# Performance work log

Hardware: AMD Instinct MI355X
Metric: run time of the kernel (lower is better)

## Reference

```python
import jax, jax.numpy as jnp
import numpy as np

V, H, B, T = 32000, 1024, 64, 512
EPS = 1e-5


def setup_inputs() -> dict:
    key = jax.random.key(0)
    ks = jax.random.split(key, 12)
    s = lambda i, shape: (jax.random.normal(ks[i], shape, dtype=jnp.float32) * 0.02)
    inp = {
        "x": jax.random.randint(ks[0], (B, T), 0, V),
        "t": jax.random.uniform(ks[1], (B,), dtype=jnp.float32),
        "emb": s(2, (V, H)),
        "w_ih1": s(3, (4 * H, H)), "w_hh1": s(4, (4 * H, H)),
        "b_ih1": jnp.zeros((4 * H,), jnp.float32), "b_hh1": jnp.zeros((4 * H,), jnp.float32),
        "gamma1": jnp.ones((H,), jnp.float32), "beta1": jnp.zeros((H,), jnp.float32),
        "w_ih2": s(5, (4 * H, H)), "w_hh2": s(6, (4 * H, H)),
        "b_ih2": jnp.zeros((4 * H,), jnp.float32), "b_hh2": jnp.zeros((4 * H,), jnp.float32),
        "gamma2": jnp.ones((H,), jnp.float32), "beta2": jnp.zeros((H,), jnp.float32),
        "fc_w": s(7, (1, H)), "fc_b": jnp.zeros((1,), jnp.float32),
        # LockedDropout: one mask per layer, reused at every timestep, pre-scaled by 1/keep
        "mask1": jax.random.bernoulli(ks[8], 0.5, (B, H)).astype(jnp.float32) / 0.5,
        "mask2": jax.random.bernoulli(ks[9], 0.7, (B, H)).astype(jnp.float32) / 0.7,
    }
    return inp


def _lstm_step(xt, h, c, w_ih, w_hh, b_ih, b_hh):
    # PyTorch LSTMCell gate order: i, f, g, o
    g = xt @ w_ih.T + h @ w_hh.T + (b_ih + b_hh)
    i, f, gg, o = jnp.split(g, 4, axis=-1)
    c = jax.nn.sigmoid(f) * c + jax.nn.sigmoid(i) * jnp.tanh(gg)
    h = jax.nn.sigmoid(o) * jnp.tanh(c)
    return h, c


def _bn(x, gamma, beta):
    # BatchNorm1d in training mode: per-feature batch stats (biased variance)
    m = x.mean(0)
    v = x.var(0)
    return gamma * (x - m) * jax.lax.rsqrt(v + EPS) + beta


def reference(x, t, emb, w_ih1, w_hh1, b_ih1, b_hh1, gamma1, beta1,
              w_ih2, w_hh2, b_ih2, b_hh2, gamma2, beta2, fc_w, fc_b,
              mask1, mask2):
    e = emb[x]                      # [B, T, H]
    e = jnp.transpose(e, (1, 0, 2)) # [T, B, H]

    def step(carry, et):
        h1, c1, h2, c2 = carry
        h1, c1 = _lstm_step(et, h1, c1, w_ih1, w_hh1, b_ih1, b_hh1)
        o = _bn(h1, gamma1, beta1) * mask1
        h2, c2 = _lstm_step(o, h2, c2, w_ih2, w_hh2, b_ih2, b_hh2)
        o = _bn(h2, gamma2, beta2) * mask2
        return (h1, c1, h2, c2), o

    z = jnp.zeros((B, H), jnp.float32)
    _, outs = jax.lax.scan(step, (z, z, z, z), e)  # outs: [T, B, H]

    pooled = outs.max(axis=0)                      # MaxPool1d over time -> [B, H]
    logits = (pooled @ fc_w.T + fc_b)[:, 0]        # [B]
    # BCEWithLogitsLoss (mean), numerically stable
    loss = jnp.mean(jnp.maximum(logits, 0.0) - logits * t + jnp.log1p(jnp.exp(-jnp.abs(logits))))
    return (loss, logits)
```

## Files before the change

### kernel.cpp

```cpp
#include <hip/hip_runtime.h>

#define HDIM  1024
#define BDIM  64
#define TDIM  512
#define FRAGB 131072
#define FRAGE 65536
#define WPAD  1032
#define SLOTS 4
#define NGRP  8

typedef __bf16 bf16x8 __attribute__((ext_vector_type(8)));
typedef float  f32x4  __attribute__((ext_vector_type(4)));
typedef int    i32x4  __attribute__((ext_vector_type(4)));

#define MFMA(a, b, c) __builtin_amdgcn_mfma_f32_16x16x32_bf16(a, b, c, 0, 0, 0)

#define GL(dst, p, off) \
    asm volatile("global_load_dwordx4 %0, %1, off offset:" off " sc0 sc1" \
                 : "=v"(dst) : "v"(p) : "memory")
#define GLF16(f, p) do { \
    const char* p0_ = (const char*)(p); \
    const char* p1_ = p0_ + 4096; const char* p2_ = p0_ + 8192; const char* p3_ = p0_ + 12288; \
    GL(f[0],  p0_, "0"); GL(f[1],  p0_, "1024"); GL(f[2],  p0_, "2048"); GL(f[3],  p0_, "3072"); \
    GL(f[4],  p1_, "0"); GL(f[5],  p1_, "1024"); GL(f[6],  p1_, "2048"); GL(f[7],  p1_, "3072"); \
    GL(f[8],  p2_, "0"); GL(f[9],  p2_, "1024"); GL(f[10], p2_, "2048"); GL(f[11], p2_, "3072"); \
    GL(f[12], p3_, "0"); GL(f[13], p3_, "1024"); GL(f[14], p3_, "2048"); GL(f[15], p3_, "3072"); \
} while (0)
#define WAITV() asm volatile("s_waitcnt vmcnt(0)" ::: "memory")
#define GS16(p, v) \
    asm volatile("global_store_dwordx4 %0, %1, off sc0 sc1" :: "v"(p), "v"(v) : "memory")

__device__ __forceinline__ float sigf(float x) { return 1.0f / (1.0f + expf(-x)); }

__device__ __forceinline__ bf16x8 cvt8(const float* p) {
    const f32x4* q = (const f32x4*)p;
    f32x4 a = q[0], b = q[1];
    bf16x8 r;
    r[0] = (__bf16)a[0]; r[1] = (__bf16)a[1]; r[2] = (__bf16)a[2]; r[3] = (__bf16)a[3];
    r[4] = (__bf16)b[0]; r[5] = (__bf16)b[1]; r[6] = (__bf16)b[2]; r[7] = (__bf16)b[3];
    return r;
}

__device__ __forceinline__ void spin2x8(const int* a, const int* b) {
    if (threadIdx.x < 64) {
        int l = threadIdx.x;
        const int* p = nullptr;
        if (l < 8)       { if (a) p = a + l * 16; }
        else if (l < 16) { if (b) p = b + (l - 8) * 16; }
        for (;;) {
            int v = 16;
            if (p) v = __hip_atomic_load(p, __ATOMIC_RELAXED, __HIP_MEMORY_SCOPE_AGENT);
            if (__all(v >= 16)) break;
            __builtin_amdgcn_s_sleep(1);
        }
    }
    __syncthreads();
}
__device__ __forceinline__ void arrive16(int* sub) {
    WAITV();
    __syncthreads();
    if (threadIdx.x == 0)
        __hip_atomic_fetch_add(sub, 1, __ATOMIC_RELAXED, __HIP_MEMORY_SCOPE_AGENT);
}
__device__ __forceinline__ void spin1(const int* c, int n) {
    if (threadIdx.x == 0)
        while (__hip_atomic_load(c, __ATOMIC_RELAXED, __HIP_MEMORY_SCOPE_AGENT) < n)
            __builtin_amdgcn_s_sleep(1);
    __syncthreads();
}

__global__ void gather_emb(const int* __restrict__ x, const float* __restrict__ emb,
                           __bf16* __restrict__ xseqfrag) {
    int t = blockIdx.x;
    for (int u = threadIdx.x; u < 8192; u += 256) {
        int lane = u & 63, c = (u >> 6) & 31, bt = u >> 11;
        int row = lane & 15, quad = lane >> 4;
        int b = bt * 16 + row, k = c * 32 + quad * 8;
        int tok = x[b * TDIM + t];
        bf16x8 r = cvt8(emb + (size_t)tok * HDIM + k);
        *(bf16x8*)(xseqfrag + (size_t)t * FRAGE + (size_t)u * 8) = r;
    }
}

__global__ void __launch_bounds__(512, 1) rnn_all(
    const int* __restrict__ x, const float* __restrict__ tv,
    const float* __restrict__ emb,
    const float* __restrict__ w_ih1, const float* __restrict__ w_hh1,
    const float* __restrict__ b_ih1, const float* __restrict__ b_hh1,
    const float* __restrict__ gamma1, const float* __restrict__ beta1,
    const float* __restrict__ w_ih2, const float* __restrict__ w_hh2,
    const float* __restrict__ b_ih2, const float* __restrict__ b_hh2,
    const float* __restrict__ gamma2, const float* __restrict__ beta2,
    const float* __restrict__ fc_w, const float* __restrict__ fc_b,
    const float* __restrict__ mask1, const float* __restrict__ mask2,
    const __bf16* __restrict__ xseq, int use_xseq,
    int* __restrict__ l1s, int* __restrict__ l2s, int* __restrict__ poolg,
    char* __restrict__ h1frag, char* __restrict__ h2frag,
    char* __restrict__ o1frag, float* __restrict__ pooled,
    float* __restrict__ out) {
    __shared__ __bf16 wih_s[32 * WPAD];
    __shared__ __bf16 whh_s[32 * WPAD];
    __shared__ float bias_s[32];
    __shared__ float gbuf[64 * 36];
    __shared__ float xh[8 * 68];
    __shared__ float stat_m[8], stat_r[8];
    __shared__ __align__(16) __bf16 hstage[512];
    __shared__ __align__(16) __bf16 ostage[512];

    const int tid   = threadIdx.x;
    const int layer = blockIdx.x & 1;
    const int lb    = blockIdx.x >> 1;
    const int grp   = lb >> 4;
    const int fbase = lb * 8;

    const float* w_ih = layer ? w_ih2 : w_ih1;
    const float* w_hh = layer ? w_hh2 : w_hh1;
    const float* b_ih = layer ? b_ih2 : b_ih1;
    const float* b_hh = layer ? b_hh2 : b_hh1;
    const float* gam_ = layer ? gamma2 : gamma1;
    const float* bet_ = layer ? beta2  : beta1;
    const float* msk_ = layer ? mask2  : mask1;

    for (int idx = tid; idx < 32 * HDIM; idx += 512) {
        int n = idx >> 10, k = idx & 1023;
        int row = (n >> 3) * HDIM + fbase + (n & 7);
        wih_s[n * WPAD + k] = (__bf16)w_ih[row * HDIM + k];
        whh_s[n * WPAD + k] = (__bf16)w_hh[row * HDIM + k];
    }
    if (tid < 32) {
        int row = (tid >> 3) * HDIM + fbase + (tid & 7);
        bias_s[tid] = b_ih[row] + b_hh[row];
    }
    __syncthreads();

    const int lane = tid & 63;
    const int wv   = tid >> 6;
    const int bt   = wv & 3;
    const int kh   = wv >> 2;
    const int qm   = lane & 15;
    const int quad = lane >> 4;
    const int kbase = kh * 512 + quad * 8;
    const int fragoff = ((bt * 32 + kh * 16) * 64 + lane) * 16;

    const __bf16* bwi0 = wih_s + qm * WPAD + kbase;
    const __bf16* bwi1 = wih_s + (16 + qm) * WPAD + kbase;
    const __bf16* bwh0 = whh_s + qm * WPAD + kbase;
    const __bf16* bwh1 = whh_s + (16 + qm) * WPAD + kbase;

    const int bb = tid >> 3, jj = tid & 7;
    const int feat = fbase + jj;
    const float gv = gam_[feat], bev = bet_[feat], mv = msk_[bb * HDIM + feat];
    float c = 0.0f, pmax = -1e30f;

    const int sbb  = tid & 63;
    const int soff = (((sbb >> 4) * 32 + (lb >> 2)) * 64 + ((lb & 3) * 16 + (sbb & 15))) * 16;

#pragma unroll 1
    for (int t = 0; t < TDIM; t++) {
        f32x4 ax0 = {0.f,0.f,0.f,0.f}, ax1 = {0.f,0.f,0.f,0.f};
        f32x4 ah0 = {0.f,0.f,0.f,0.f}, ah1 = {0.f,0.f,0.f,0.f};
        bf16x8 fh[16];

        if (layer == 0) {
            if (use_xseq) {
                const __bf16* a = xseq + (size_t)t * FRAGE + (fragoff >> 1);
#pragma unroll 4
                for (int i = 0; i < 16; i++) {
                    bf16x8 va = *(const bf16x8*)(a + i * 512);
                    ax0 = MFMA(va, *(const bf16x8*)(bwi0 + i * 32), ax0);
                    ax1 = MFMA(va, *(const bf16x8*)(bwi1 + i * 32), ax1);
                }
            } else {
                const float* a = emb + (size_t)x[(bt * 16 + qm) * TDIM + t] * HDIM + kbase;
#pragma unroll 4
                for (int i = 0; i < 16; i++) {
                    bf16x8 va = cvt8(a + i * 32);
                    ax0 = MFMA(va, *(const bf16x8*)(bwi0 + i * 32), ax0);
                    ax1 = MFMA(va, *(const bf16x8*)(bwi1 + i * 32), ax1);
                }
            }
            spin2x8(t >= 1 ? l1s + (size_t)(t - 1) * NGRP * 16 : nullptr,
                    t >= SLOTS ? l2s + (size_t)(t - SLOTS) * NGRP * 16 : nullptr);
            GLF16(fh, h1frag + (size_t)(t & 1) * FRAGB + fragoff);
            WAITV();
#pragma unroll
            for (int i = 0; i < 16; i++) {
                ah0 = MFMA(fh[i], *(const bf16x8*)(bwh0 + i * 32), ah0);
                ah1 = MFMA(fh[i], *(const bf16x8*)(bwh1 + i * 32), ah1);
            }
        } else {
            spin2x8(l1s + (size_t)t * NGRP * 16,
                    t >= 1 ? l2s + (size_t)(t - 1) * NGRP * 16 : nullptr);
            bf16x8 fo[16];
            GLF16(fo, o1frag + (size_t)(t & (SLOTS - 1)) * FRAGB + fragoff);
            GLF16(fh, h2frag + (size_t)(t & 1) * FRAGB + fragoff);
            WAITV();
#pragma unroll
            for (int i = 0; i < 16; i++) {
                ax0 = MFMA(fo[i], *(const bf16x8*)(bwi0 + i * 32), ax0);
                ax1 = MFMA(fo[i], *(const bf16x8*)(bwi1 + i * 32), ax1);
                ah0 = MFMA(fh[i], *(const bf16x8*)(bwh0 + i * 32), ah0);
                ah1 = MFMA(fh[i], *(const bf16x8*)(bwh1 + i * 32), ah1);
            }
        }

        if (kh == 0) {
#pragma unroll
            for (int r = 0; r < 4; r++) {
                int row = (bt * 16 + quad * 4 + r) * 36;
                gbuf[row + qm]      = ax0[r] + ah0[r] + bias_s[qm];
                gbuf[row + 16 + qm] = ax1[r] + ah1[r] + bias_s[16 + qm];
            }
        }
        __syncthreads();
        if (kh == 1) {
#pragma unroll
            for (int r = 0; r < 4; r++) {
                int row = (bt * 16 + quad * 4 + r) * 36;
                gbuf[row + qm]      += ax0[r] + ah0[r];
                gbuf[row + 16 + qm] += ax1[r] + ah1[r];
            }
        }
        __syncthreads();

        float gi = gbuf[bb * 36 + jj];
        float gf = gbuf[bb * 36 + 8 + jj];
        float gg = gbuf[bb * 36 + 16 + jj];
        float go = gbuf[bb * 36 + 24 + jj];
        c = sigf(gf) * c + sigf(gi) * tanhf(gg);
        float h = sigf(go) * tanhf(c);
        hstage[tid] = (__bf16)h;
        xh[jj * 68 + bb] = h;
        __syncthreads();
        float v = xh[wv * 68 + lane];
        float s1 = v, s2 = v * v;
#pragma unroll
        for (int off = 32; off; off >>= 1) {
            s1 += __shfl_xor(s1, off);
            s2 += __shfl_xor(s2, off);
        }
        if (lane == 0) {
            float m  = s1 * (1.0f / 64.0f);
            float va = s2 * (1.0f / 64.0f) - m * m;
            stat_m[wv] = m;
            stat_r[wv] = rsqrtf(va + 1e-5f);
        }
        __syncthreads();
        float o = ((h - stat_m[jj]) * stat_r[jj] * gv + bev) * mv;
        if (layer == 0) ostage[tid] = (__bf16)o;
        else            pmax = fmaxf(pmax, o);
        __syncthreads();

        if (layer == 0) {
            if (tid < 64) {
                i32x4 val = *(const i32x4*)(hstage + tid * 8);
                GS16(h1frag + (size_t)((t + 1) & 1) * FRAGB + soff, val);
            } else if (tid < 128) {
                i32x4 val = *(const i32x4*)(ostage + (tid - 64) * 8);
                GS16(o1frag + (size_t)(t & (SLOTS - 1)) * FRAGB + soff, val);
            }
            arrive16(l1s + ((size_t)t * NGRP + grp) * 16);
        } else {
            if (tid < 64) {
                i32x4 val = *(const i32x4*)(hstage + tid * 8);
                GS16(h2frag + (size_t)((t + 1) & 1) * FRAGB + soff, val);
            }
            arrive16(l2s + ((size_t)t * NGRP + grp) * 16);
        }
    }

    if (layer == 1) {
        __hip_atomic_store(&pooled[bb * HDIM + feat], pmax,
                           __ATOMIC_RELAXED, __HIP_MEMORY_SCOPE_AGENT);
        WAITV();
        __syncthreads();
        if (tid == 0)
            __hip_atomic_fetch_add(poolg, 1, __ATOMIC_RELAXED, __HIP_MEMORY_SCOPE_AGENT);

        if (lb == 0) {
            spin1(poolg, 128);
            __builtin_amdgcn_fence(__ATOMIC_ACQUIRE, "agent");
            int b  = wv * 8 + (lane >> 3);
            int l8 = lane & 7;
            float s = 0.0f;
            for (int f = l8 * 128; f < l8 * 128 + 128; f++)
                s += pooled[b * HDIM + f] * fc_w[f];
            s += __shfl_xor(s, 1); s += __shfl_xor(s, 2); s += __shfl_xor(s, 4);
            float logit = s + fc_b[0];
            if (l8 == 0) {
                out[1 + b] = logit;
                gbuf[b] = fmaxf(logit, 0.0f) - logit * tv[b] + log1pf(expf(-fabsf(logit)));
            }
            __syncthreads();
            if (tid < 64) {
                float term = gbuf[tid];
#pragma unroll
                for (int off = 32; off; off >>= 1) term += __shfl_xor(term, off);
                if (tid == 0) out[0] = term * (1.0f / 64.0f);
            }
        }
    }
}

extern "C" void kernel_launch(void* const* d_in, const int* in_sizes, int n_in,
                              void* d_out, int out_size, void* d_ws, size_t ws_size,
                              hipStream_t stream) {
    const int*   x    = (const int*)d_in[0];
    const float* tv   = (const float*)d_in[1];
    const float* emb  = (const float*)d_in[2];
    const float* wih1 = (const float*)d_in[3];
    const float* whh1 = (const float*)d_in[4];
    const float* bih1 = (const float*)d_in[5];
    const float* bhh1 = (const float*)d_in[6];
    const float* g1   = (const float*)d_in[7];
    const float* be1  = (const float*)d_in[8];
    const float* wih2 = (const float*)d_in[9];
    const float* whh2 = (const float*)d_in[10];
    const float* bih2 = (const float*)d_in[11];
    const float* bhh2 = (const float*)d_in[12];
    const float* g2   = (const float*)d_in[13];
    const float* be2  = (const float*)d_in[14];
    const float* fcw  = (const float*)d_in[15];
    const float* fcb  = (const float*)d_in[16];
    const float* m1   = (const float*)d_in[17];
    const float* m2   = (const float*)d_in[18];

    char* w = (char*)d_ws;
    int*    l1s    = (int*)(w);
    int*    l2s    = (int*)(w + 262144);
    int*    poolg  = (int*)(w + 524288);
    char*   h1frag = w + 528384;
    char*   h2frag = w + 528384 + 262144;
    char*   o1frag = w + 1052672;
    float*  pooled = (float*)(w + 1576960);
    __bf16* xseq   = (__bf16*)(w + 1839104);
    float*  out    = (float*)d_out;

    size_t need_xseq = (size_t)1839104 + (size_t)TDIM * FRAGB;
    int use_xseq = (ws_size >= need_xseq) ? 1 : 0;

    hipMemsetAsync(d_ws, 0, 1052672, stream);

    if (use_xseq)
        gather_emb<<<dim3(TDIM), dim3(256), 0, stream>>>(x, emb, xseq);

    void* args[] = {&x, &tv, &emb, &wih1, &whh1, &bih1, &bhh1, &g1, &be1,
                    &wih2, &whh2, &bih2, &bhh2, &g2, &be2, &fcw, &fcb, &m1, &m2,
                    &xseq, &use_xseq,
                    &l1s, &l2s, &poolg,
                    &h1frag, &h2frag, &o1frag, &pooled, &out};
    hipLaunchCooperativeKernel((void*)rnn_all, dim3(256), dim3(512), args, 0, stream);
}
```

Baseline: 4.306 ms.

## Use full per-timestep history buffers to drop slot-reuse waits and cache-bypassing loads

When the workspace is large enough, h1, h2 and o1 fragments are written into a separate slot for every timestep instead of ring buffers. Layer 1 then no longer has to wait for layer 2 to free a slot. Because each address is written only once, the loads switch from sc0/sc1 cache-bypassing inline asm to plain loads after an acquire fence. The LDS weight row padding also changes. In exchange the workspace use grows greatly, and correctness now depends on visibility through the spin flag plus fence, which is risky if plain loads can hit stale cache lines.

```diff
diff --git a/kernel.cpp b/kernel.cpp
--- a/kernel.cpp
+++ b/kernel.cpp
@@ -5,7 +5,7 @@
 #define TDIM  512
 #define FRAGB 131072
 #define FRAGE 65536
-#define WPAD  1032
+#define WPAD  1048
 #define SLOTS 4
 #define NGRP  8
 
@@ -41,6 +41,11 @@
     return r;
 }
 
+__device__ __forceinline__ void load16c(bf16x8* f, const char* p) {
+#pragma unroll
+    for (int i = 0; i < 16; i++) f[i] = *(const bf16x8*)(p + i * 1024);
+}
+
 __device__ __forceinline__ void spin2x8(const int* a, const int* b) {
     if (threadIdx.x < 64) {
         int l = threadIdx.x;
@@ -82,6 +87,7 @@
     }
 }
 
+template <int BIG>
 __global__ void __launch_bounds__(512, 1) rnn_all(
     const int* __restrict__ x, const float* __restrict__ tv,
     const float* __restrict__ emb,
@@ -95,9 +101,9 @@
     const float* __restrict__ mask1, const float* __restrict__ mask2,
     const __bf16* __restrict__ xseq, int use_xseq,
     int* __restrict__ l1s, int* __restrict__ l2s, int* __restrict__ poolg,
-    char* __restrict__ h1frag, char* __restrict__ h2frag,
-    char* __restrict__ o1frag, float* __restrict__ pooled,
-    float* __restrict__ out) {
+    const char* __restrict__ hzero,
+    char* __restrict__ h1p, char* __restrict__ h2p, char* __restrict__ o1p,
+    float* __restrict__ pooled, float* __restrict__ out) {
     __shared__ __bf16 wih_s[32 * WPAD];
     __shared__ __bf16 whh_s[32 * WPAD];
     __shared__ float bias_s[32];
@@ -132,6 +138,8 @@
         bias_s[tid] = b_ih[row] + b_hh[row];
     }
     __syncthreads();
+    if (BIG)
+        __builtin_amdgcn_fence(__ATOMIC_ACQUIRE, "agent");
 
     const int lane = tid & 63;
     const int wv   = tid >> 6;
@@ -179,22 +187,36 @@
                     ax1 = MFMA(va, *(const bf16x8*)(bwi1 + i * 32), ax1);
                 }
             }
-            spin2x8(t >= 1 ? l1s + (size_t)(t - 1) * NGRP * 16 : nullptr,
-                    t >= SLOTS ? l2s + (size_t)(t - SLOTS) * NGRP * 16 : nullptr);
-            GLF16(fh, h1frag + (size_t)(t & 1) * FRAGB + fragoff);
-            WAITV();
+            if (BIG) {
+                spin2x8(t >= 1 ? l1s + (size_t)(t - 1) * NGRP * 16 : nullptr, nullptr);
+                const char* src = (t == 0) ? hzero : h1p + (size_t)(t - 1) * FRAGB;
+                load16c(fh, src + fragoff);
+            } else {
+                spin2x8(t >= 1 ? l1s + (size_t)(t - 1) * NGRP * 16 : nullptr,
+                        t >= SLOTS ? l2s + (size_t)(t - SLOTS) * NGRP * 16 : nullptr);
+                GLF16(fh, h1p + (size_t)(t & 1) * FRAGB + fragoff);
+                WAITV();
+            }
 #pragma unroll
             for (int i = 0; i < 16; i++) {
                 ah0 = MFMA(fh[i], *(const bf16x8*)(bwh0 + i * 32), ah0);
                 ah1 = MFMA(fh[i], *(const bf16x8*)(bwh1 + i * 32), ah1);
             }
         } else {
-            spin2x8(l1s + (size_t)t * NGRP * 16,
-                    t >= 1 ? l2s + (size_t)(t - 1) * NGRP * 16 : nullptr);
             bf16x8 fo[16];
-            GLF16(fo, o1frag + (size_t)(t & (SLOTS - 1)) * FRAGB + fragoff);
-            GLF16(fh, h2frag + (size_t)(t & 1) * FRAGB + fragoff);
-            WAITV();
+            if (BIG) {
+                spin2x8(l1s + (size_t)t * NGRP * 16,
+                        t >= 1 ? l2s + (size_t)(t - 1) * NGRP * 16 : nullptr);
+                load16c(fo, o1p + (size_t)t * FRAGB + fragoff);
+                const char* src = (t == 0) ? hzero : h2p + (size_t)(t - 1) * FRAGB;
+                load16c(fh, src + fragoff);
+            } else {
+                spin2x8(l1s + (size_t)t * NGRP * 16,
+                        t >= 1 ? l2s + (size_t)(t - 1) * NGRP * 16 : nullptr);
+                GLF16(fo, o1p + (size_t)(t & (SLOTS - 1)) * FRAGB + fragoff);
+                GLF16(fh, h2p + (size_t)(t & 1) * FRAGB + fragoff);
+                WAITV();
+            }
 #pragma unroll
             for (int i = 0; i < 16; i++) {
                 ax0 = MFMA(fo[i], *(const bf16x8*)(bwi0 + i * 32), ax0);
@@ -252,18 +274,21 @@
         __syncthreads();
 
         if (layer == 0) {
+            size_t hslot = BIG ? (size_t)t * FRAGB : (size_t)((t + 1) & 1) * FRAGB;
+            size_t oslot = BIG ? (size_t)t * FRAGB : (size_t)(t & (SLOTS - 1)) * FRAGB;
             if (tid < 64) {
                 i32x4 val = *(const i32x4*)(hstage + tid * 8);
-                GS16(h1frag + (size_t)((t + 1) & 1) * FRAGB + soff, val);
+                GS16(h1p + hslot + soff, val);
             } else if (tid < 128) {
                 i32x4 val = *(const i32x4*)(ostage + (tid - 64) * 8);
-                GS16(o1frag + (size_t)(t & (SLOTS - 1)) * FRAGB + soff, val);
+                GS16(o1p + oslot + soff, val);
             }
             arrive16(l1s + ((size_t)t * NGRP + grp) * 16);
         } else {
+            size_t hslot = BIG ? (size_t)t * FRAGB : (size_t)((t + 1) & 1) * FRAGB;
             if (tid < 64) {
                 i32x4 val = *(const i32x4*)(hstage + tid * 8);
-                GS16(h2frag + (size_t)((t + 1) & 1) * FRAGB + soff, val);
+                GS16(h2p + hslot + soff, val);
             }
             arrive16(l2s + ((size_t)t * NGRP + grp) * 16);
         }
@@ -326,28 +351,55 @@
     const float* m2   = (const float*)d_in[18];
 
     char* w = (char*)d_ws;
+    float* out = (float*)d_out;
+
+    const size_t SEQB = (size_t)TDIM * FRAGB;
+    size_t boff = 0;
+    int*   B_l1s   = (int*)(w + boff); boff += 262144;
+    int*   B_l2s   = (int*)(w + boff); boff += 262144;
+    int*   B_poolg = (int*)(w + boff); boff += 4096;
+    char*  B_hzero = w + boff;         boff += FRAGB;
+    size_t B_msz   = boff;
+    char*  B_h1    = w + boff;         boff += SEQB;
+    char*  B_h2    = w + boff;         boff += SEQB;
+    char*  B_o1    = w + boff;         boff += SEQB;
+    float* B_pool  = (float*)(w + boff); boff += 262144;
+    __bf16* B_xseq = (__bf16*)(w + boff); boff += SEQB;
+    size_t need_big = boff;
+
+    if (ws_size >= need_big) {
+        hipMemsetAsync(d_ws, 0, B_msz, stream);
+        gather_emb<<<dim3(TDIM), dim3(256), 0, stream>>>(x, emb, B_xseq);
+        int use_xseq = 1;
+        void* args[] = {&x, &tv, &emb, &wih1, &whh1, &bih1, &bhh1, &g1, &be1,
+                        &wih2, &whh2, &bih2, &bhh2, &g2, &be2, &fcw, &fcb, &m1, &m2,
+                        (void*)&B_xseq, &use_xseq,
+                        &B_l1s, &B_l2s, &B_poolg, (void*)&B_hzero,
+                        &B_h1, &B_h2, &B_o1, &B_pool, &out};
+        hipLaunchCooperativeKernel((void*)rnn_all<1>, dim3(256), dim3(512), args, 0, stream);
+        return;
+    }
+
     int*    l1s    = (int*)(w);
     int*    l2s    = (int*)(w + 262144);
     int*    poolg  = (int*)(w + 524288);
-    char*   h1frag = w + 528384;
-    char*   h2frag = w + 528384 + 262144;
-    char*   o1frag = w + 1052672;
-    float*  pooled = (float*)(w + 1576960);
-    __bf16* xseq   = (__bf16*)(w + 1839104);
-    float*  out    = (float*)d_out;
-
-    size_t need_xseq = (size_t)1839104 + (size_t)TDIM * FRAGB;
-    int use_xseq = (ws_size >= need_xseq) ? 1 : 0;
-
-    hipMemsetAsync(d_ws, 0, 1052672, stream);
-
+    char*   hzero  = w + 524288 + 4096;
+    char*   h1frag = w + 528384 + FRAGB;
+    char*   h2frag = h1frag + 262144;
+    char*   o1frag = h2frag + 262144;
+    float*  pooled = (float*)(o1frag + 524288);
+    __bf16* xseq   = (__bf16*)((char*)pooled + 262144);
+    size_t fixed   = (size_t)((char*)xseq - w);
+    int use_xseq = (ws_size >= fixed + SEQB) ? 1 : 0;
+
+    hipMemsetAsync(d_ws, 0, fixed, stream);
     if (use_xseq)
         gather_emb<<<dim3(TDIM), dim3(256), 0, stream>>>(x, emb, xseq);
 
     void* args[] = {&x, &tv, &emb, &wih1, &whh1, &bih1, &bhh1, &g1, &be1,
                     &wih2, &whh2, &bih2, &bhh2, &g2, &be2, &fcw, &fcb, &m1, &m2,
-                    &xseq, &use_xseq,
-                    &l1s, &l2s, &poolg,
+                    (void*)&xseq, &use_xseq,
+                    &l1s, &l2s, &poolg, (void*)&hzero,
                     &h1frag, &h2frag, &o1frag, &pooled, &out};
-    hipLaunchCooperativeKernel((void*)rnn_all, dim3(256), dim3(512), args, 0, stream);
-}
+    hipLaunchCooperativeKernel((void*)rnn_all<0>, dim3(256), dim3(512), args, 0, stream);
+}
```

Measured after the change: 4.070 ms. 1.06x faster.
